# Performance work log

Hardware: AMD Instinct MI355X
Metric: run time of the kernel (lower is better)

## Reference

```python
import jax, jax.numpy as jnp
import numpy as np

B, C, H, W = 4, 128, 256, 256
MID = W // 2
V = H * W
N_ROUNDS = 17   # >= ceil(log2(V)); Boruvka halves component count per round
N_DOUBLE = 17   # pointer-doubling steps to fully flatten parent chains
BIG = jnp.int32(2 ** 30)
EPS = 1e-8      # torch.cosine_similarity default eps


def build_edges(h, w):
    """Replicates _build_matrix_index: 4-connected edges inside each half + cross edges."""
    raw = (jnp.arange(w, dtype=jnp.int32)[None, :]
           + jnp.arange(h, dtype=jnp.int32)[:, None] * w)          # [H, W]
    mid = w // 2
    L, R = raw[:, :mid], raw[:, mid:]

    def pairs(a, b):
        return jnp.stack([a.reshape(-1), b.reshape(-1)], axis=1)

    e = jnp.concatenate([
        pairs(L[:-1, :], L[1:, :]),   # left rows
        pairs(L[:, :-1], L[:, 1:]),   # left cols
        pairs(R[:-1, :], R[1:, :]),   # right rows
        pairs(R[:, :-1], R[:, 1:]),   # right cols
        pairs(L, R),                  # cross (bi) edges
    ], axis=0)                        # [E, 2]
    return e[:, 0], e[:, 1]


def cosine_weights(fm):
    """Replicates _build_feature_weight_cosine (mapping_func=None, max_tree=False)."""
    b, c = fm.shape[0], fm.shape[1]
    fl, fr = fm[:, :, :, :MID], fm[:, :, :, MID:]

    def cos(a, bb):  # a, bb: [B, C, N] -> [B, N]
        a = a.reshape(b, c, -1)
        bb = bb.reshape(b, c, -1)
        dot = jnp.sum(a * bb, axis=1)
        na = jnp.sqrt(jnp.sum(a * a, axis=1))
        nb = jnp.sqrt(jnp.sum(bb * bb, axis=1))
        return dot / jnp.maximum(na * nb, EPS)

    return jnp.concatenate([
        cos(fl[:, :, :-1, :], fl[:, :, 1:, :]),
        cos(fl[:, :, :, :-1], fl[:, :, :, 1:]),
        cos(fr[:, :, :-1, :], fr[:, :, 1:, :]),
        cos(fr[:, :, :, :-1], fr[:, :, :, 1:]),
        cos(fl, fr),
    ], axis=1)                        # [B, E]


def mst_boruvka(u, v, w):
    """Parallel Boruvka minimum spanning tree. Returns bool mask [E] of selected edges.
    Deterministic tie-break via global weight rank (unique integer keys)."""
    E = w.shape[0]
    order = jnp.argsort(w)
    rank = jnp.zeros(E, jnp.int32).at[order].set(jnp.arange(E, dtype=jnp.int32))
    ids = jnp.arange(V, dtype=jnp.int32)

    def find_root(p):
        return jax.lax.fori_loop(0, N_DOUBLE, lambda i, q: q[q], p)

    def round_fn(i, state):
        parent, selected = state
        root = find_root(parent)
        ru, rv = root[u], root[v]
        valid = ru != rv
        key = jnp.where(valid, rank, BIG)
        # cheapest outgoing edge per component (either endpoint)
        min_u = jax.ops.segment_min(key, ru, num_segments=V)
        min_v = jax.ops.segment_min(key, rv, num_segments=V)
        comp_min = jnp.minimum(min_u, min_v)          # [V]
        win_u = valid & (key == comp_min[ru])
        win_v = valid & (key == comp_min[rv])
        selected = selected | win_u | win_v
        # hook winning components onto the other endpoint's root (drop non-winners)
        p1 = root.at[jnp.where(win_u, ru, jnp.int32(V))].set(rv, mode='drop')
        p2 = p1.at[jnp.where(win_v, rv, jnp.int32(V))].set(ru, mode='drop')
        # break 2-cycles deterministically
        cyc = (p2[p2] == ids) & (ids < p2)
        parent = jnp.where(cyc, ids, p2)
        return (parent, selected)

    parent0 = ids
    sel0 = jnp.zeros(E, dtype=bool)
    _, selected = jax.lax.fori_loop(0, N_ROUNDS, round_fn, (parent0, sel0))
    return selected


def setup_inputs() -> dict:
    key = jax.random.key(0)
    guide_in = jax.random.normal(key, (B, C, H, W), dtype=jnp.float32)
    return {"guide_in": guide_in}


def reference(guide_in):
    u, v = build_edges(H, W)                # shared across batch
    w = cosine_weights(guide_in)            # [B, E]
    sel = jax.vmap(lambda wb: mst_boruvka(u, v, wb))(w)  # [B, E] bool
    # emulate _C.mst_forward output as the selected-edge mask (V-1 trues per image)
    return sel.astype(jnp.float32)
```

## Files before the change

### kernel.cpp

```cpp
#include <hip/hip_runtime.h>
#include <stdint.h>

namespace {

typedef unsigned long long ull;
constexpr int B = 4, C = 128, H = 256, W = 256;
constexpr int V = H * W;
constexpr int E = 163072;
constexpr long long CHW = (long long)C * V;
constexpr int ROUNDS = 17;
constexpr int NBLKV = (B * V) / 256;
constexpr int SEG = 768;

__device__ __forceinline__ void edge_uv(int e, int& u, int& v) {
  if (e < 32640) {
    int h = e >> 7, w = e & 127;
    u = (h << 8) + w; v = u + 256;
  } else if (e < 65152) {
    int k = e - 32640; int h = k / 127, w = k - h * 127;
    u = (h << 8) + w; v = u + 1;
  } else if (e < 97792) {
    int k = e - 65152; int h = k >> 7, w = k & 127;
    u = (h << 8) + 128 + w; v = u + 256;
  } else if (e < 130304) {
    int k = e - 97792; int h = k / 127, w = k - h * 127;
    u = (h << 8) + 128 + w; v = u + 1;
  } else {
    int k = e - 130304; int h = k >> 7, w = k & 127;
    u = (h << 8) + w; v = u + 128;
  }
}

__device__ __forceinline__ int find_root(const int* __restrict__ par, int v) {
  int cur = v;
  int p = par[cur];
  for (int g = 0; g < 70000 && p != cur; ++g) {
    int gp = par[p];
    if (gp == cur) { cur = cur < p ? cur : p; break; }
    cur = p; p = gp;
  }
  return cur;
}

__global__ void k_weight3(const float* __restrict__ x, ull* __restrict__ wkey,
                          float* __restrict__ out) {
  int idx = blockIdx.x * blockDim.x + threadIdx.x;
  int b = idx >> 15, rem = idx & 32767;
  int h = rem >> 7, q = rem & 127;
  int w0 = q << 1;
  bool isL  = q < 64;
  bool hasV = h < 255;
  int voff = hasV ? 256 : 0;
  int roff = (isL ? (q < 63) : (q < 127)) ? 2 : 0;

  const float* xb = x + (long long)b * CHW + (h << 8) + w0;
  double n0x = 0, n0y = 0, ndnx = 0, ndny = 0, nrtx = 0, ncrx = 0, ncry = 0;
  double dv0 = 0, dv1 = 0, dh0 = 0, dh1 = 0, dx0 = 0, dx1 = 0;
  if (isL) {
#pragma unroll 4
    for (int c = 0; c < C; ++c) {
      const float* pc = xb + (long long)c * V;
      float2 a  = *(const float2*)pc;
      float2 dn = *(const float2*)(pc + voff);
      float2 rt = *(const float2*)(pc + roff);
      float2 cr = *(const float2*)(pc + 128);
      double ax = a.x, ay = a.y, dnx = dn.x, dny = dn.y, rtx = rt.x,
             crx = cr.x, cry = cr.y;
      n0x = fma(ax, ax, n0x);   n0y = fma(ay, ay, n0y);
      ndnx = fma(dnx, dnx, ndnx); ndny = fma(dny, dny, ndny);
      nrtx = fma(rtx, rtx, nrtx);
      ncrx = fma(crx, crx, ncrx); ncry = fma(cry, cry, ncry);
      dv0 = fma(ax, dnx, dv0);  dv1 = fma(ay, dny, dv1);
      dh0 = fma(ax, ay, dh0);   dh1 = fma(ay, rtx, dh1);
      dx0 = fma(ax, crx, dx0);  dx1 = fma(ay, cry, dx1);
    }
  } else {
#pragma unroll 4
    for (int c = 0; c < C; ++c) {
      const float* pc = xb + (long long)c * V;
      float2 a  = *(const float2*)pc;
      float2 dn = *(const float2*)(pc + voff);
      float2 rt = *(const float2*)(pc + roff);
      double ax = a.x, ay = a.y, dnx = dn.x, dny = dn.y, rtx = rt.x;
      n0x = fma(ax, ax, n0x);   n0y = fma(ay, ay, n0y);
      ndnx = fma(dnx, dnx, ndnx); ndny = fma(dny, dny, ndny);
      nrtx = fma(rtx, rtx, nrtx);
      dv0 = fma(ax, dnx, dv0);  dv1 = fma(ay, dny, dv1);
      dh0 = fma(ax, ay, dh0);   dh1 = fma(ay, rtx, dh1);
    }
  }

  ull* wk = wkey + (size_t)b * E;
  float* ob = out + (size_t)b * E;
  auto emit = [&](int e, double nu, double nv, double dot) {
    double denom = fmax(sqrt(nu) * sqrt(nv), 1e-8);
    float wv = (float)(dot / denom);
    unsigned int bits = __float_as_uint(wv);
    if (wv == 0.0f) bits = 0u;
    unsigned int mapped = bits ^ (((int)bits < 0) ? 0xFFFFFFFFu : 0x80000000u);
    wk[e] = ((ull)mapped << 32) | (unsigned int)e;
    ob[e] = 0.0f;
  };
  if (isL) {
    if (hasV) {
      emit((h << 7) + w0,     n0x, ndnx, dv0);
      emit((h << 7) + w0 + 1, n0y, ndny, dv1);
    }
    emit(32640 + h * 127 + w0, n0x, n0y, dh0);
    if (q < 63) emit(32640 + h * 127 + w0 + 1, n0y, nrtx, dh1);
    emit(130304 + (h << 7) + w0,     n0x, ncrx, dx0);
    emit(130304 + (h << 7) + w0 + 1, n0y, ncry, dx1);
  } else {
    int wr = w0 - 128;
    if (hasV) {
      emit(65152 + (h << 7) + wr,     n0x, ndnx, dv0);
      emit(65152 + (h << 7) + wr + 1, n0y, ndny, dv1);
    }
    emit(97792 + h * 127 + wr, n0x, n0y, dh0);
    if (q < 127) emit(97792 + h * 127 + wr + 1, n0y, nrtx, dh1);
  }
}

__global__ void k_r0(const ull* __restrict__ wkey, ull* __restrict__ minE0,
                     ull* __restrict__ minE1, int* __restrict__ parent,
                     float* __restrict__ out, int* __restrict__ flags) {
  int idx = blockIdx.x * blockDim.x + threadIdx.x;
  int b = idx >> 16, v = idx & (V - 1);
  int h = v >> 8, w = v & 255;
  bool isL = w < 128;
  int wl = isL ? w : w - 128;
  int vb = isL ? 0 : 65152, hb = isL ? 32640 : 97792;
  const ull* wk = wkey + (size_t)b * E;
  ull m = ~0ULL;
  if (h > 0)    m = min(m, wk[vb + ((h - 1) << 7) + wl]);
  if (h < 255)  m = min(m, wk[vb + (h << 7) + wl]);
  if (wl > 0)   m = min(m, wk[hb + h * 127 + wl - 1]);
  if (wl < 127) m = min(m, wk[hb + h * 127 + wl]);
  m = min(m, wk[130304 + (h << 7) + wl]);
  int e = (int)(m & 0xFFFFFFFFu);
  int eu, ev; edge_uv(e, eu, ev);
  out[(size_t)b * E + e] = 1.0f;
  parent[idx] = (v == eu) ? ev : eu;
  minE0[idx] = ~0ULL;
  minE1[idx] = ~0ULL;
  if (idx < 32) flags[idx] = (idx <= 2) ? 1 : 0;
}

__global__ void k_root(const int* __restrict__ parent, int* __restrict__ root) {
  int idx = blockIdx.x * blockDim.x + threadIdx.x;
  int b = idx >> 16;
  root[idx] = find_root(parent + (b << 16), idx & (V - 1));
}

__global__ void k_vminR1(const int* __restrict__ root, const ull* __restrict__ wkey,
                         ull* __restrict__ minE) {
  int idx = blockIdx.x * blockDim.x + threadIdx.x;
  int b = idx >> 16, v = idx & (V - 1);
  int h = v >> 8, w = v & 255;
  bool isL = w < 128;
  int wl = isL ? w : w - 128;
  int vb = isL ? 0 : 65152, hb = isL ? 32640 : 97792;
  const int* rt = root + (b << 16);
  const ull* wk = wkey + (size_t)b * E;
  int rme = rt[v];
  ull m = ~0ULL;
  if (h > 0    && rt[v - 256] != rme) m = min(m, wk[vb + ((h - 1) << 7) + wl]);
  if (h < 255  && rt[v + 256] != rme) m = min(m, wk[vb + (h << 7) + wl]);
  if (wl > 0   && rt[v - 1]   != rme) m = min(m, wk[hb + h * 127 + wl - 1]);
  if (wl < 127 && rt[v + 1]   != rme) m = min(m, wk[hb + h * 127 + wl]);
  int xn = isL ? v + 128 : v - 128;
  if (rt[xn] != rme) m = min(m, wk[130304 + (h << 7) + wl]);
  if (m != ~0ULL) atomicMin(minE + (b << 16) + rme, m);
}

__global__ void k_vminR2(const int* __restrict__ root, const ull* __restrict__ wkey,
                         ull* __restrict__ minE,
                         int* __restrict__ elseg, int* __restrict__ cntblk) {
  __shared__ int lcnt;
  if (threadIdx.x == 0) lcnt = 0;
  __syncthreads();
  int idx = blockIdx.x * blockDim.x + threadIdx.x;
  int b = idx >> 16, v = idx & (V - 1);
  int h = v >> 8, w = v & 255;
  bool isL = w < 128;
  int wl = isL ? w : w - 128;
  int vb = isL ? 0 : 65152, hb = isL ? 32640 : 97792;
  const int* rt = root + (b << 16);
  const ull* wk = wkey + (size_t)b * E;
  int rme = rt[v];
  ull m = ~0ULL;
  int base = blockIdx.x * SEG;
  if (h > 0   && rt[v - 256] != rme) m = min(m, wk[vb + ((h - 1) << 7) + wl]);
  if (wl > 0  && rt[v - 1]   != rme) m = min(m, wk[hb + h * 127 + wl - 1]);
  if (!isL    && rt[v - 128] != rme) m = min(m, wk[130304 + (h << 7) + wl]);
  if (h < 255 && rt[v + 256] != rme) {
    int e = vb + (h << 7) + wl;
    m = min(m, wk[e]);
    elseg[base + atomicAdd(&lcnt, 1)] = e;
  }
  if (wl < 127 && rt[v + 1] != rme) {
    int e = hb + h * 127 + wl;
    m = min(m, wk[e]);
    elseg[base + atomicAdd(&lcnt, 1)] = e;
  }
  if (isL && rt[v + 128] != rme) {
    int e = 130304 + (h << 7) + wl;
    m = min(m, wk[e]);
    elseg[base + atomicAdd(&lcnt, 1)] = e;
  }
  if (m != ~0ULL) atomicMin(minE + (b << 16) + rme, m);
  __syncthreads();
  if (threadIdx.x == 0) cntblk[blockIdx.x] = lcnt;
}

__global__ void k_hookV(ull* __restrict__ minE, const int* __restrict__ root,
                        int* __restrict__ parent, float* __restrict__ out) {
  int idx = blockIdx.x * blockDim.x + threadIdx.x;
  int b = idx >> 16, v = idx & (V - 1);
  int rr = root[idx];
  int np = rr;
  if (rr == v) {
    ull k = minE[idx];
    if (k != ~0ULL) {
      int e = (int)(k & 0xFFFFFFFFu);
      int eu, ev; edge_uv(e, eu, ev);
      const int* rt = root + (b << 16);
      int ru = rt[eu], rv2 = rt[ev];
      out[(size_t)b * E + e] = 1.0f;
      np = (v == ru) ? rv2 : ru;
      minE[idx] = ~0ULL;
    }
  }
  int* par = parent + (b << 16);
  if (par[v] != np) par[v] = np;
}

__global__ void k_edgeA(int* __restrict__ parent, const ull* __restrict__ wkey,
                        ull* __restrict__ mcur, int* __restrict__ elseg,
                        unsigned int* __restrict__ prblk, int* __restrict__ cntblk,
                        int* __restrict__ flags, int r) {
  if (__hip_atomic_load(flags + r - 1, __ATOMIC_RELAXED,
                        __HIP_MEMORY_SCOPE_AGENT) == 0)
    return;
  int j = blockIdx.x, t = threadIdx.x;
  int n = cntblk[j];
  if (n == 0) return;
  __shared__ int lcnt;
  if (t == 0) lcnt = 0;
  int b = j >> 8;
  int* par = parent + (b << 16);
  const ull* wk = wkey + (size_t)b * E;
  ull* mb = mcur + (b << 16);
  int base = j * SEG;
  int se[3]; unsigned int sp[3]; int ns = 0;
#pragma unroll
  for (int it = 0; it < 3; ++it) {
    int i = t + (it << 8);
    if (i < n) {
      int e = elseg[base + i];
      int u, v; edge_uv(e, u, v);
      int ru = find_root(par, u);
      int rv = find_root(par, v);
      if (par[u] != ru) par[u] = ru;
      if (par[v] != rv) par[v] = rv;
      if (ru != rv) {
        ull k = wk[e];
        atomicMin(mb + ru, k);
        atomicMin(mb + rv, k);
        se[ns] = e;
        sp[ns] = ((unsigned int)ru << 16) | (unsigned int)rv;
        ++ns;
      }
    }
  }
  __syncthreads();
  for (int i2 = 0; i2 < ns; ++i2) {
    int pos = atomicAdd(&lcnt, 1);
    elseg[base + pos] = se[i2];
    prblk[base + pos] = sp[i2];
  }
  __syncthreads();
  if (t == 0) {
    cntblk[j] = lcnt;
    if (lcnt &&
        __hip_atomic_load(flags + r, __ATOMIC_RELAXED, __HIP_MEMORY_SCOPE_AGENT) == 0)
      __hip_atomic_fetch_or(flags + r, 1, __ATOMIC_RELAXED, __HIP_MEMORY_SCOPE_AGENT);
  }
}

__global__ void k_edgeB(const ull* __restrict__ mcur, ull* __restrict__ mnext,
                        const int* __restrict__ elseg,
                        const unsigned int* __restrict__ prblk,
                        const int* __restrict__ cntblk,
                        int* __restrict__ parent, float* __restrict__ out,
                        const int* __restrict__ flags, int r) {
  if (__hip_atomic_load(flags + r, __ATOMIC_RELAXED,
                        __HIP_MEMORY_SCOPE_AGENT) == 0)
    return;
  int j = blockIdx.x, t = threadIdx.x;
  int n = cntblk[j];
  if (n == 0) return;
  int b = j >> 8;
  const ull* mbc = mcur + (b << 16);
  ull* mbn = mnext + (b << 16);
  int* par = parent + (b << 16);
  float* ob = out + (size_t)b * E;
  int base = j * SEG;
  for (int i = t; i < n; i += 256) {
    int e = elseg[base + i];
    unsigned int pr = prblk[base + i];
    int ru = (int)(pr >> 16), rv = (int)(pr & 0xFFFFu);
    ull mu = mbc[ru];
    ull mv = mbc[rv];
    bool wu = ((int)(mu & 0xFFFFFFFFu) == e);
    bool wv = ((int)(mv & 0xFFFFFFFFu) == e);
    if (wu | wv) ob[e] = 1.0f;
    if (wu) par[ru] = rv;
    if (wv) par[rv] = ru;
    mbn[ru] = ~0ULL;
    mbn[rv] = ~0ULL;
  }
}

__global__ __launch_bounds__(1024)
void k_endgame(int* __restrict__ parent, ull* __restrict__ minE,
               const ull* __restrict__ wkey, float* __restrict__ out,
               const int* __restrict__ elseg, const int* __restrict__ cntblk,
               int* __restrict__ fe, unsigned int* __restrict__ fr) {
  int b = blockIdx.x, t = threadIdx.x;
  const ull* wk = wkey + (size_t)b * E;
  ull* mb = minE + (b << 16);
  int* par = parent + (b << 16);
  float* ob = out + (size_t)b * E;
  int* feb = fe + (size_t)b * E;
  unsigned int* frb = fr + (size_t)b * E;

  __shared__ int pre[257];
  __shared__ int wofs[16];
  __shared__ int s_wc;

  if (t == 0) pre[0] = 0;
  if (t < 256) pre[t + 1] = cntblk[(b << 8) + t];
  __syncthreads();
  for (int ofs = 1; ofs < 256; ofs <<= 1) {
    int cur = 0, add = 0;
    if (t < 256) { cur = pre[t + 1]; if (t + 1 > ofs) add = pre[t + 1 - ofs]; }
    __syncthreads();
    if (t < 256) pre[t + 1] = cur + add;
    __syncthreads();
  }
  if (t < 256) {
    int dst = pre[t], cnt2 = pre[t + 1] - dst;
    int src = ((b << 8) + t) * SEG;
    for (int i = 0; i < cnt2; ++i) feb[dst + i] = elseg[src + i];
  }
  __syncthreads();
  int n = pre[256];

  for (int round = 9; round < ROUNDS && n > 0; ++round) {
    if (t == 0) s_wc = 0;
    __syncthreads();
    for (int base = 0; base < n; base += 1024) {
      int i = base + t;
      bool keep = false; int e = 0; unsigned int pr = 0;
      if (i < n) {
        e = feb[i];
        int u, v; edge_uv(e, u, v);
        int ru = find_root(par, u);
        int rv = find_root(par, v);
        if (par[u] != ru) par[u] = ru;
        if (par[v] != rv) par[v] = rv;
        if (ru != rv) {
          keep = true;
          pr = ((unsigned int)ru << 16) | (unsigned int)rv;
          ull k = wk[e];
          atomicMin(mb + ru, k);
          atomicMin(mb + rv, k);
        }
      }
      ull msk = __ballot(keep);
      int lane = t & 63, wid = t >> 6;
      if (lane == 0) wofs[wid] = (int)__popcll(msk);
      __syncthreads();
      if (t == 0) {
        int s = s_wc;
#pragma unroll
        for (int k2 = 0; k2 < 16; ++k2) { int c2 = wofs[k2]; wofs[k2] = s; s += c2; }
        s_wc = s;
      }
      __syncthreads();
      if (keep) {
        int pos = wofs[wid] + (int)__popcll(msk & ((1ULL << lane) - 1));
        feb[pos] = e;
        frb[pos] = pr;
      }
    }
    __syncthreads();
    int kept = s_wc;
    for (int i = t; i < kept; i += 1024) {
      unsigned int pr = frb[i];
      int ru = (int)(pr >> 16), rv = (int)(pr & 0xFFFFu);
      int e = feb[i];
      ull mu = __hip_atomic_load(mb + ru, __ATOMIC_RELAXED, __HIP_MEMORY_SCOPE_AGENT);
      ull mv = __hip_atomic_load(mb + rv, __ATOMIC_RELAXED, __HIP_MEMORY_SCOPE_AGENT);
      bool wu = ((int)(mu & 0xFFFFFFFFu) == e);
      bool wv = ((int)(mv & 0xFFFFFFFFu) == e);
      if (wu | wv) ob[e] = 1.0f;
      if (wu) par[ru] = rv;
      if (wv) par[rv] = ru;
    }
    __syncthreads();
    for (int i = t; i < kept; i += 1024) {
      unsigned int pr = frb[i];
      __hip_atomic_store(mb + (int)(pr >> 16), ~0ULL, __ATOMIC_RELAXED,
                         __HIP_MEMORY_SCOPE_AGENT);
      __hip_atomic_store(mb + (int)(pr & 0xFFFFu), ~0ULL, __ATOMIC_RELAXED,
                         __HIP_MEMORY_SCOPE_AGENT);
    }
    n = kept;
    __syncthreads();
  }
}

}

extern "C" void kernel_launch(void* const* d_in, const int* in_sizes, int n_in,
                              void* d_out, int out_size, void* d_ws, size_t ws_size,
                              hipStream_t stream) {
  const float* x = (const float*)d_in[0];
  float* out = (float*)d_out;

  char* ws = (char*)d_ws;
  size_t off = 0;
  auto alloc = [&](size_t bytes) {
    void* p = (void*)(ws + off);
    off += (bytes + 255) & ~(size_t)255;
    return p;
  };
  int* parent = (int*)alloc((size_t)B * V * sizeof(int));
  int* root   = (int*)alloc((size_t)B * V * sizeof(int));
  ull* minE0  = (ull*)alloc((size_t)B * V * 8);
  ull* minE1  = (ull*)alloc((size_t)B * V * 8);
  ull* wkey   = (ull*)alloc((size_t)B * E * 8);
  int* elseg  = (int*)alloc((size_t)NBLKV * SEG * sizeof(int));
  unsigned int* prblk = (unsigned int*)alloc((size_t)NBLKV * SEG * 4);
  int* cntblk = (int*)alloc((size_t)NBLKV * sizeof(int));
  int* flags  = (int*)alloc(32 * sizeof(int));
  int* fe     = (int*)alloc((size_t)B * E * sizeof(int));
  unsigned int* fr = (unsigned int*)alloc((size_t)B * E * 4);

  k_weight3<<<(B * H * 128) / 512, 512, 0, stream>>>(x, wkey, out);
  k_r0     <<<(B * V) / 1024, 1024, 0, stream>>>(wkey, minE0, minE1, parent, out, flags);

  k_root  <<<(B * V) / 1024, 1024, 0, stream>>>(parent, root);
  k_vminR1<<<(B * V) / 1024, 1024, 0, stream>>>(root, wkey, minE0);
  k_hookV <<<(B * V) / 1024, 1024, 0, stream>>>(minE0, root, parent, out);

  k_root  <<<(B * V) / 1024, 1024, 0, stream>>>(parent, root);
  k_vminR2<<<NBLKV, 256, 0, stream>>>(root, wkey, minE0, elseg, cntblk);
  k_hookV <<<(B * V) / 1024, 1024, 0, stream>>>(minE0, root, parent, out);

  for (int r = 3; r <= 8; ++r) {
    ull* mcur  = (r & 1) ? minE0 : minE1;
    ull* mnext = (r & 1) ? minE1 : minE0;
    k_edgeA<<<NBLKV, 256, 0, stream>>>(parent, wkey, mcur, elseg, prblk,
                                       cntblk, flags, r);
    k_edgeB<<<NBLKV, 256, 0, stream>>>(mcur, mnext, elseg, prblk, cntblk,
                                       parent, out, flags, r);
  }

  k_endgame<<<B, 1024, 0, stream>>>(parent, minE0, wkey, out, elseg, cntblk, fe, fr);
}
```

Before: 245.0 us.

## Stage input rows through LDS tiles in cosine weight kernel

The weight kernel now processes four image rows per block and, for every group of four channels, cooperatively loads five rows (the four plus a halo row below) into shared memory. Neighbor loads for the down, right and cross edges are then served from LDS. This targets redundant global reads, since each row was previously fetched twice (as a row and as another row's down neighbor). The cost is two barriers per channel group and 20KB of LDS per block, which may lower occupancy and limit how much load latency can overlap.

Result: no change. 247.8 us (+1.2%).

```diff
diff --git a/kernel.cpp b/kernel.cpp
--- a/kernel.cpp
+++ b/kernel.cpp
@@ -42,51 +42,63 @@
   return cur;
 }
 
-__global__ void k_weight3(const float* __restrict__ x, ull* __restrict__ wkey,
-                          float* __restrict__ out) {
-  int idx = blockIdx.x * blockDim.x + threadIdx.x;
-  int b = idx >> 15, rem = idx & 32767;
-  int h = rem >> 7, q = rem & 127;
+__global__ __launch_bounds__(512)
+void k_weight_t(const float* __restrict__ x, ull* __restrict__ wkey,
+                float* __restrict__ out) {
+  __shared__ float lds[4 * 5 * 256];
+  int blk = blockIdx.x;
+  int b = blk >> 6;
+  int h0 = (blk & 63) << 2;
+  int t = threadIdx.x;
+  int row = t >> 7, q = t & 127;
+  int h = h0 + row;
   int w0 = q << 1;
   bool isL  = q < 64;
   bool hasV = h < 255;
-  int voff = hasV ? 256 : 0;
   int roff = (isL ? (q < 63) : (q < 127)) ? 2 : 0;
-
-  const float* xb = x + (long long)b * CHW + (h << 8) + w0;
+  int drow = hasV ? row + 1 : row;
+
+  const float* xb = x + (long long)b * CHW;
   double n0x = 0, n0y = 0, ndnx = 0, ndny = 0, nrtx = 0, ncrx = 0, ncry = 0;
   double dv0 = 0, dv1 = 0, dh0 = 0, dh1 = 0, dx0 = 0, dx1 = 0;
-  if (isL) {
-#pragma unroll 4
-    for (int c = 0; c < C; ++c) {
-      const float* pc = xb + (long long)c * V;
-      float2 a  = *(const float2*)pc;
-      float2 dn = *(const float2*)(pc + voff);
-      float2 rt = *(const float2*)(pc + roff);
-      float2 cr = *(const float2*)(pc + 128);
-      double ax = a.x, ay = a.y, dnx = dn.x, dny = dn.y, rtx = rt.x,
-             crx = cr.x, cry = cr.y;
-      n0x = fma(ax, ax, n0x);   n0y = fma(ay, ay, n0y);
-      ndnx = fma(dnx, dnx, ndnx); ndny = fma(dny, dny, ndny);
-      nrtx = fma(rtx, rtx, nrtx);
-      ncrx = fma(crx, crx, ncrx); ncry = fma(cry, cry, ncry);
-      dv0 = fma(ax, dnx, dv0);  dv1 = fma(ay, dny, dv1);
-      dh0 = fma(ax, ay, dh0);   dh1 = fma(ay, rtx, dh1);
-      dx0 = fma(ax, crx, dx0);  dx1 = fma(ay, cry, dx1);
-    }
-  } else {
-#pragma unroll 4
-    for (int c = 0; c < C; ++c) {
-      const float* pc = xb + (long long)c * V;
-      float2 a  = *(const float2*)pc;
-      float2 dn = *(const float2*)(pc + voff);
-      float2 rt = *(const float2*)(pc + roff);
-      double ax = a.x, ay = a.y, dnx = dn.x, dny = dn.y, rtx = rt.x;
-      n0x = fma(ax, ax, n0x);   n0y = fma(ay, ay, n0y);
-      ndnx = fma(dnx, dnx, ndnx); ndny = fma(dny, dny, ndny);
-      nrtx = fma(rtx, rtx, nrtx);
-      dv0 = fma(ax, dnx, dv0);  dv1 = fma(ay, dny, dv1);
-      dh0 = fma(ax, ay, dh0);   dh1 = fma(ay, rtx, dh1);
+
+  for (int c0 = 0; c0 < C; c0 += 4) {
+    __syncthreads();
+#pragma unroll
+    for (int i = 0; i < 10; ++i) {
+      int f = (i << 9) + t;
+      int ci = f / 1280, rem = f - ci * 1280;
+      int rr = rem >> 8, ww = rem & 255;
+      int gh = h0 + rr; if (gh > 255) gh = 255;
+      lds[f] = xb[(long long)(c0 + ci) * V + (gh << 8) + ww];
+    }
+    __syncthreads();
+#pragma unroll
+    for (int cc = 0; cc < 4; ++cc) {
+      const float* base   = &lds[cc * 1280 + (row << 8)];
+      const float* basedn = &lds[cc * 1280 + (drow << 8)];
+      float2 a  = *(const float2*)(base + w0);
+      float2 dn = *(const float2*)(basedn + w0);
+      float2 rt = *(const float2*)(base + w0 + roff);
+      if (isL) {
+        float2 cr = *(const float2*)(base + w0 + 128);
+        double ax = a.x, ay = a.y, dnx = dn.x, dny = dn.y, rtx = rt.x,
+               crx = cr.x, cry = cr.y;
+        n0x = fma(ax, ax, n0x);   n0y = fma(ay, ay, n0y);
+        ndnx = fma(dnx, dnx, ndnx); ndny = fma(dny, dny, ndny);
+        nrtx = fma(rtx, rtx, nrtx);
+        ncrx = fma(crx, crx, ncrx); ncry = fma(cry, cry, ncry);
+        dv0 = fma(ax, dnx, dv0);  dv1 = fma(ay, dny, dv1);
+        dh0 = fma(ax, ay, dh0);   dh1 = fma(ay, rtx, dh1);
+        dx0 = fma(ax, crx, dx0);  dx1 = fma(ay, cry, dx1);
+      } else {
+        double ax = a.x, ay = a.y, dnx = dn.x, dny = dn.y, rtx = rt.x;
+        n0x = fma(ax, ax, n0x);   n0y = fma(ay, ay, n0y);
+        ndnx = fma(dnx, dnx, ndnx); ndny = fma(dny, dny, ndny);
+        nrtx = fma(rtx, rtx, nrtx);
+        dv0 = fma(ax, dnx, dv0);  dv1 = fma(ay, dny, dv1);
+        dh0 = fma(ax, ay, dh0);   dh1 = fma(ay, rtx, dh1);
+      }
     }
   }
 
@@ -449,7 +461,7 @@
   int* fe     = (int*)alloc((size_t)B * E * sizeof(int));
   unsigned int* fr = (unsigned int*)alloc((size_t)B * E * 4);
 
-  k_weight3<<<(B * H * 128) / 512, 512, 0, stream>>>(x, wkey, out);
+  k_weight_t<<<B * (H / 4), 512, 0, stream>>>(x, wkey, out);
   k_r0     <<<(B * V) / 1024, 1024, 0, stream>>>(wkey, minE0, minE1, parent, out, flags);
 
   k_root  <<<(B * V) / 1024, 1024, 0, stream>>>(parent, root);
```
